# Optimization experiments

Hardware: AMD Instinct MI355X
Metric: run time of the kernel (lower is better)

## Reference

```python
import jax, jax.numpy as jnp
import numpy as np

N_NODES = 100000
N_EDGES = 3200000
N_FEAT = 512
HIDDEN = 16
N_CLASS = 7


def gcn_conv(x, edge_index, W, b, n_nodes):
    """PyG GCNConv (add_self_loops=True, symmetric normalization).
    x: [N, F_in]; edge_index: [2, E] with row=source, col=target.
    """
    h = x @ W  # [N, F_out] -- linear transform before aggregation (F_out small)
    src, dst = edge_index[0], edge_index[1]
    # degree computed on target column (incl. self-loop), as in PyG gcn_norm
    deg = jax.ops.segment_sum(jnp.ones(src.shape[0], dtype=h.dtype), dst,
                              num_segments=n_nodes) + 1.0
    dinv = jax.lax.rsqrt(deg)  # deg >= 1 always (self-loops)
    norm = dinv[src] * dinv[dst]  # [E]
    msg = norm[:, None] * h[src]  # [E, F_out]
    agg = jax.ops.segment_sum(msg, dst, num_segments=n_nodes)
    # self-loop contribution: norm_ii = dinv_i^2
    agg = agg + (dinv * dinv)[:, None] * h
    return agg + b


def setup_inputs() -> dict:
    key = jax.random.key(0)
    k1, k2, k3, k4 = jax.random.split(key, 4)
    x = jax.random.normal(k1, (N_NODES, N_FEAT), dtype=jnp.float32)
    edge_index = jax.random.randint(k2, (2, N_EDGES), 0, N_NODES, dtype=jnp.int64)
    W1 = jax.random.normal(k3, (N_FEAT, HIDDEN), dtype=jnp.float32) * (1.0 / np.sqrt(N_FEAT))
    b1 = jnp.zeros((HIDDEN,), dtype=jnp.float32)
    W2 = jax.random.normal(k4, (HIDDEN, N_CLASS), dtype=jnp.float32) * (1.0 / np.sqrt(HIDDEN))
    b2 = jnp.zeros((N_CLASS,), dtype=jnp.float32)
    return {"x": x, "edge_index": edge_index, "W1": W1, "b1": b1, "W2": W2, "b2": b2}


def reference(x, edge_index, W1, b1, W2, b2):
    n = x.shape[0]
    h = gcn_conv(x, edge_index, W1, b1, n)
    h = jax.nn.relu(h)
    # F.dropout in eval mode is identity (deterministic reference)
    h = gcn_conv(h, edge_index, W2, b2, n)
    return jax.nn.log_softmax(h, axis=1)
```

## Files before the change

kernel.cpp:

```cpp
#include <hip/hip_runtime.h>
#include <math.h>


#define F_IN 512
#define HID  16
#define NCLS 7
#define NCHUNK 256
#define BK 64
#define NBMAX 1600
#define CAP 3072

static __device__ __forceinline__ float bf2f(unsigned short u) {
    union { unsigned int i; float f; } v; v.i = ((unsigned int)u) << 16; return v.f;
}
static __device__ __forceinline__ unsigned short f2bf(float f) {
    union { float f; unsigned int u; } v; v.f = f;
    unsigned int b = v.u;
    return (unsigned short)((b + 0x7FFFu + ((b >> 16) & 1u)) >> 16);
}

__global__ __launch_bounds__(256) void k_a1(const int* __restrict__ ei, int E, int perChunk,
                                            int nb, int* __restrict__ bh) {
    __shared__ int hist[NBMAX];
    for (int t = threadIdx.x; t < nb; t += 256) hist[t] = 0;
    __syncthreads();
    const int* dst = ei + E;
    int c = blockIdx.x;
    int s0 = c * perChunk;
    int s1 = min(s0 + perChunk, E);
    for (int e = s0 + threadIdx.x; e < s1; e += 256)
        atomicAdd(&hist[dst[e] >> 6], 1);
    __syncthreads();
    for (int t = threadIdx.x; t < nb; t += 256) bh[(size_t)c * nb + t] = hist[t];
}

__global__ __launch_bounds__(256) void k_a2a(int* __restrict__ bh, int nb,
                                             int* __restrict__ Tb) {
    __shared__ int sd[256];
    int b = blockIdx.x, tid = threadIdx.x;
    int v = bh[(size_t)tid * nb + b];
    sd[tid] = v;
    __syncthreads();
    for (int off = 1; off < 256; off <<= 1) {
        int t = (tid >= off) ? sd[tid - off] : 0;
        __syncthreads();
        sd[tid] += t;
        __syncthreads();
    }
    bh[(size_t)tid * nb + b] = sd[tid] - v;
    if (tid == 255) Tb[b] = sd[255];
}

__global__ __launch_bounds__(256) void k_a2b(const int* __restrict__ Tb, int nb,
                                             int* __restrict__ Bb) {
    __shared__ int sd[256];
    int tid = threadIdx.x;
    int carry = 0;
    for (int base = 0; base < nb; base += 256) {
        int v = (base + tid < nb) ? Tb[base + tid] : 0;
        sd[tid] = v;
        __syncthreads();
        for (int off = 1; off < 256; off <<= 1) {
            int t = (tid >= off) ? sd[tid - off] : 0;
            __syncthreads();
            sd[tid] += t;
            __syncthreads();
        }
        if (base + tid < nb) Bb[base + tid] = carry + sd[tid] - v;
        carry += sd[255];
        __syncthreads();
    }
}

__global__ __launch_bounds__(256) void k_a3(const int* __restrict__ ei, int E, int perChunk,
                                            int nb, const int* __restrict__ bh,
                                            const int* __restrict__ Bb,
                                            unsigned* __restrict__ part) {
    __shared__ int cur[NBMAX];
    __shared__ int baseL[NBMAX];
    int c = blockIdx.x;
    for (int t = threadIdx.x; t < nb; t += 256) {
        cur[t] = 0;
        baseL[t] = Bb[t] + bh[(size_t)c * nb + t];
    }
    __syncthreads();
    const int* src = ei;
    const int* dst = ei + E;
    int s0 = c * perChunk;
    int s1 = min(s0 + perChunk, E);
    for (int e = s0 + threadIdx.x; e < s1; e += 256) {
        int s = src[e], d = dst[e];
        int b = d >> 6;
        int r = atomicAdd(&cur[b], 1);
        part[baseL[b] + r] = ((unsigned)(d & (BK - 1)) << 20) | (unsigned)s;
    }
}

__global__ __launch_bounds__(256) void k_b(const unsigned* __restrict__ part,
                                           const int* __restrict__ Tb,
                                           const int* __restrict__ Bb,
                                           int* __restrict__ csr, int* __restrict__ cnt,
                                           int* __restrict__ offs, float* __restrict__ dinv,
                                           int N) {
    __shared__ unsigned eL[CAP];
    __shared__ int hist[BK], sd[BK], cur[BK];
    int b = blockIdx.x, tid = threadIdx.x;
    int base = Bb[b], ct = Tb[b];
    if (tid < BK) hist[tid] = 0;
    __syncthreads();
    for (int k = tid; k < ct; k += 256) {
        unsigned v = part[base + k];
        if (k < CAP) eL[k] = v;
        atomicAdd(&hist[v >> 20], 1);
    }
    __syncthreads();
    if (tid < BK) sd[tid] = hist[tid];
    __syncthreads();
    for (int off = 1; off < BK; off <<= 1) {
        int t = 0;
        if (tid < BK && tid >= off) t = sd[tid - off];
        __syncthreads();
        if (tid < BK) sd[tid] += t;
        __syncthreads();
    }
    if (tid < BK) {
        int h = hist[tid];
        int ex = sd[tid] - h;
        cur[tid] = ex;
        int node = b * BK + tid;
        if (node < N) {
            cnt[node] = h;
            offs[node] = base + ex;
            dinv[node] = rsqrtf((float)h + 1.0f);
        }
    }
    __syncthreads();
    for (int k = tid; k < ct; k += 256) {
        unsigned v = (k < CAP) ? eL[k] : part[base + k];
        int dl = (int)(v >> 20);
        int r = atomicAdd(&cur[dl], 1);
        csr[base + r] = (int)(v & 0xFFFFFu);
    }
}

__global__ __launch_bounds__(256) void k_gemm1(const float* __restrict__ x,
                                               const float* __restrict__ W1,
                                               const float* __restrict__ dinv,
                                               unsigned short* __restrict__ hs1b,
                                               int N, int halfN) {
    __shared__ float wl[F_IN * HID];
    for (int t = threadIdx.x; t < F_IN * HID; t += 256) wl[t] = W1[t];
    __syncthreads();
    int gid = blockIdx.x * blockDim.x + threadIdx.x;
    if (gid >= halfN) return;
    int r0 = gid, r1 = gid + halfN;
    bool has1 = (r1 < N);
    const float* x0 = x + (size_t)r0 * F_IN;
    const float* x1 = has1 ? (x + (size_t)r1 * F_IN) : x0;
    float acc0[HID], acc1[HID];
#pragma unroll
    for (int j = 0; j < HID; j++) { acc0[j] = 0.0f; acc1[j] = 0.0f; }
    for (int k0 = 0; k0 < F_IN; k0 += 4) {
        float4 a = *(const float4*)(x0 + k0);
        float4 bq = *(const float4*)(x1 + k0);
        const float* w0 = &wl[k0 * HID];
#pragma unroll
        for (int j = 0; j < HID; j++) {
            float w = w0[j];
            acc0[j] = fmaf(a.x, w, acc0[j]); acc1[j] = fmaf(bq.x, w, acc1[j]);
        }
#pragma unroll
        for (int j = 0; j < HID; j++) {
            float w = w0[HID + j];
            acc0[j] = fmaf(a.y, w, acc0[j]); acc1[j] = fmaf(bq.y, w, acc1[j]);
        }
#pragma unroll
        for (int j = 0; j < HID; j++) {
            float w = w0[2 * HID + j];
            acc0[j] = fmaf(a.z, w, acc0[j]); acc1[j] = fmaf(bq.z, w, acc1[j]);
        }
#pragma unroll
        for (int j = 0; j < HID; j++) {
            float w = w0[3 * HID + j];
            acc0[j] = fmaf(a.w, w, acc0[j]); acc1[j] = fmaf(bq.w, w, acc1[j]);
        }
    }
    float d0 = dinv[r0];
    unsigned p0[8];
#pragma unroll
    for (int j = 0; j < 8; j++) {
        unsigned lo = f2bf(d0 * acc0[2 * j]);
        unsigned hi = f2bf(d0 * acc0[2 * j + 1]);
        p0[j] = lo | (hi << 16);
    }
    *(uint4*)(hs1b + (size_t)r0 * HID)     = make_uint4(p0[0], p0[1], p0[2], p0[3]);
    *(uint4*)(hs1b + (size_t)r0 * HID + 8) = make_uint4(p0[4], p0[5], p0[6], p0[7]);
    if (has1) {
        float d1 = dinv[r1];
        unsigned p1[8];
#pragma unroll
        for (int j = 0; j < 8; j++) {
            unsigned lo = f2bf(d1 * acc1[2 * j]);
            unsigned hi = f2bf(d1 * acc1[2 * j + 1]);
            p1[j] = lo | (hi << 16);
        }
        *(uint4*)(hs1b + (size_t)r1 * HID)     = make_uint4(p1[0], p1[1], p1[2], p1[3]);
        *(uint4*)(hs1b + (size_t)r1 * HID + 8) = make_uint4(p1[4], p1[5], p1[6], p1[7]);
    }
}

__global__ __launch_bounds__(256) void k_agg1(const int* __restrict__ csr,
                                              const int* __restrict__ offs,
                                              const int* __restrict__ cnt,
                                              const float* __restrict__ dinv,
                                              const unsigned short* __restrict__ hs1b,
                                              const float* __restrict__ b1,
                                              const float* __restrict__ W2,
                                              float* __restrict__ hs2, int N) {
    int lane = threadIdx.x & 15;
    int i = blockIdx.x * 16 + (threadIdx.x >> 4);
    float w2r[NCLS];
#pragma unroll
    for (int c = 0; c < NCLS; c++) w2r[c] = W2[lane * NCLS + c];
    float b1l = b1[lane];
    if (i >= N) return;
    int start = offs[i], end = start + cnt[i];
    float acc = bf2f(hs1b[(size_t)i * HID + lane]);
    int k = start;
    for (; k + 3 < end; k += 4) {
        int s0 = csr[k], s1 = csr[k + 1], s2 = csr[k + 2], s3 = csr[k + 3];
        float v0 = bf2f(hs1b[(size_t)s0 * HID + lane]);
        float v1 = bf2f(hs1b[(size_t)s1 * HID + lane]);
        float v2 = bf2f(hs1b[(size_t)s2 * HID + lane]);
        float v3 = bf2f(hs1b[(size_t)s3 * HID + lane]);
        acc += (v0 + v1) + (v2 + v3);
    }
    for (; k < end; k++)
        acc += bf2f(hs1b[(size_t)csr[k] * HID + lane]);
    float v = fmaf(dinv[i], acc, b1l);
    float hr = v > 0.0f ? v : 0.0f;
    float dv = dinv[i];
    float res[NCLS];
#pragma unroll
    for (int c = 0; c < NCLS; c++) {
        float t = hr * w2r[c];
#pragma unroll
        for (int w = 8; w >= 1; w >>= 1) t += __shfl_xor(t, w, 16);
        res[c] = t;
    }
    if (lane < NCLS) {
        float o = res[0];
#pragma unroll
        for (int c = 1; c < NCLS; c++) o = (lane == c) ? res[c] : o;
        hs2[(size_t)i * NCLS + lane] = dv * o;
    }
}

__global__ __launch_bounds__(256) void k_agg2(const int* __restrict__ csr,
                                              const int* __restrict__ offs,
                                              const int* __restrict__ cnt,
                                              const float* __restrict__ dinv,
                                              const float* __restrict__ hs2,
                                              const float* __restrict__ b2,
                                              float* __restrict__ out, int N) {
    int lane = threadIdx.x & 7;
    int i = blockIdx.x * 32 + (threadIdx.x >> 3);
    if (i >= N) return;
    int cc = lane < NCLS ? lane : NCLS - 1;
    int start = offs[i], end = start + cnt[i];
    float acc = hs2[(size_t)i * NCLS + cc];
    int k = start;
    for (; k + 3 < end; k += 4) {
        int s0 = csr[k], s1 = csr[k + 1], s2 = csr[k + 2], s3 = csr[k + 3];
        float v0 = hs2[(size_t)s0 * NCLS + cc];
        float v1 = hs2[(size_t)s1 * NCLS + cc];
        float v2 = hs2[(size_t)s2 * NCLS + cc];
        float v3 = hs2[(size_t)s3 * NCLS + cc];
        acc += (v0 + v1) + (v2 + v3);
    }
    for (; k < end; k++)
        acc += hs2[(size_t)csr[k] * NCLS + cc];
    float v = fmaf(dinv[i], acc, b2[cc]);
    float vm = (lane < NCLS) ? v : -INFINITY;
    float m = vm;
#pragma unroll
    for (int w = 4; w >= 1; w >>= 1) m = fmaxf(m, __shfl_xor(m, w, 8));
    float e = (lane < NCLS) ? expf(v - m) : 0.0f;
    float ssum = e;
#pragma unroll
    for (int w = 4; w >= 1; w >>= 1) ssum += __shfl_xor(ssum, w, 8);
    if (lane < NCLS) out[(size_t)i * NCLS + lane] = v - m - logf(ssum);
}

extern "C" void kernel_launch(void* const* d_in, const int* in_sizes, int n_in,
                              void* d_out, int out_size, void* d_ws, size_t ws_size,
                              hipStream_t stream) {
    const float* x  = (const float*)d_in[0];
    const int*   ei = (const int*)d_in[1];
    const float* W1 = (const float*)d_in[2];
    const float* b1 = (const float*)d_in[3];
    const float* W2 = (const float*)d_in[4];
    const float* b2 = (const float*)d_in[5];
    float* out = (float*)d_out;

    const int N = in_sizes[0] / F_IN;
    const int E = in_sizes[1] / 2;
    const int nb = (N + BK - 1) / BK;
    const int halfN = (N + 1) / 2;
    const int perChunk = (E + NCHUNK - 1) / NCHUNK;

    unsigned* w = (unsigned*)d_ws;
    auto al4 = [](size_t v) { return (v + 3) & ~(size_t)3; };
    size_t o = 0;
    unsigned*       part = w + o;               o = al4(o + E);
    int*            csr  = (int*)(w + o);       o = al4(o + E);
    unsigned short* hs1b = (unsigned short*)(w + o); o = al4(o + (size_t)N * HID / 2);
    float*          hs2  = (float*)(w + o);     o = al4(o + (size_t)N * NCLS);
    float*          dinv = (float*)(w + o);     o = al4(o + N);
    int*            cnt  = (int*)(w + o);       o = al4(o + N);
    int*            offs = (int*)(w + o);       o = al4(o + N);
    int*            bh   = (int*)(w + o);       o = al4(o + (size_t)NCHUNK * nb);
    int*            Tb   = (int*)(w + o);       o = al4(o + nb);
    int*            Bb   = (int*)(w + o);

    k_a1<<<NCHUNK, 256, 0, stream>>>(ei, E, perChunk, nb, bh);
    k_a2a<<<nb, 256, 0, stream>>>(bh, nb, Tb);
    k_a2b<<<1, 256, 0, stream>>>(Tb, nb, Bb);
    k_a3<<<NCHUNK, 256, 0, stream>>>(ei, E, perChunk, nb, bh, Bb, part);
    k_b<<<nb, 256, 0, stream>>>(part, Tb, Bb, csr, cnt, offs, dinv, N);
    k_gemm1<<<(halfN + 255) / 256, 256, 0, stream>>>(x, W1, dinv, hs1b, N, halfN);
    k_agg1<<<(N + 15) / 16, 256, 0, stream>>>(csr, offs, cnt, dinv, hs1b, b1, W2, hs2, N);
    k_agg2<<<(N + 31) / 32, 256, 0, stream>>>(csr, offs, cnt, dinv, hs2, b2, out, N);
}
```

Before: 513.8 us.

## Restructure GEMM1 so 16-lane groups split K with coalesced row loads

The first linear layer now assigns 16 lanes to each group of 4 rows. Each lane reads a contiguous float4 slice of the row and multiplies it against a transposed, padded copy of W1 in shared memory. Partial sums are combined with a butterfly shuffle reduction that leaves one output column per lane. This replaces one-thread-per-two-rows loads, which strided 2KB per lane, with coalesced accesses to the large x matrix. The cost is shuffle-reduction overhead and scalar bf16 stores, plus a messy host-side workspace layout recomputation.

Result: faster. 486.7 us (-5.3%).

```diff
diff --git a/kernel.cpp b/kernel.cpp
--- a/kernel.cpp
+++ b/kernel.cpp
@@ -9,6 +9,7 @@
 #define BK 64
 #define NBMAX 1600
 #define CAP 3072
+#define WT_STRIDE 516
 
 static __device__ __forceinline__ float bf2f(unsigned short u) {
     union { unsigned int i; float f; } v; v.i = ((unsigned int)u) << 16; return v.f;
@@ -147,65 +148,83 @@
                                                const float* __restrict__ W1,
                                                const float* __restrict__ dinv,
                                                unsigned short* __restrict__ hs1b,
-                                               int N, int halfN) {
-    __shared__ float wl[F_IN * HID];
-    for (int t = threadIdx.x; t < F_IN * HID; t += 256) wl[t] = W1[t];
-    __syncthreads();
-    int gid = blockIdx.x * blockDim.x + threadIdx.x;
-    if (gid >= halfN) return;
-    int r0 = gid, r1 = gid + halfN;
-    bool has1 = (r1 < N);
-    const float* x0 = x + (size_t)r0 * F_IN;
-    const float* x1 = has1 ? (x + (size_t)r1 * F_IN) : x0;
-    float acc0[HID], acc1[HID];
-#pragma unroll
-    for (int j = 0; j < HID; j++) { acc0[j] = 0.0f; acc1[j] = 0.0f; }
-    for (int k0 = 0; k0 < F_IN; k0 += 4) {
-        float4 a = *(const float4*)(x0 + k0);
-        float4 bq = *(const float4*)(x1 + k0);
-        const float* w0 = &wl[k0 * HID];
-#pragma unroll
-        for (int j = 0; j < HID; j++) {
-            float w = w0[j];
-            acc0[j] = fmaf(a.x, w, acc0[j]); acc1[j] = fmaf(bq.x, w, acc1[j]);
-        }
-#pragma unroll
-        for (int j = 0; j < HID; j++) {
-            float w = w0[HID + j];
-            acc0[j] = fmaf(a.y, w, acc0[j]); acc1[j] = fmaf(bq.y, w, acc1[j]);
-        }
-#pragma unroll
-        for (int j = 0; j < HID; j++) {
-            float w = w0[2 * HID + j];
-            acc0[j] = fmaf(a.z, w, acc0[j]); acc1[j] = fmaf(bq.z, w, acc1[j]);
-        }
-#pragma unroll
-        for (int j = 0; j < HID; j++) {
-            float w = w0[3 * HID + j];
-            acc0[j] = fmaf(a.w, w, acc0[j]); acc1[j] = fmaf(bq.w, w, acc1[j]);
-        }
-    }
-    float d0 = dinv[r0];
-    unsigned p0[8];
-#pragma unroll
-    for (int j = 0; j < 8; j++) {
-        unsigned lo = f2bf(d0 * acc0[2 * j]);
-        unsigned hi = f2bf(d0 * acc0[2 * j + 1]);
-        p0[j] = lo | (hi << 16);
-    }
-    *(uint4*)(hs1b + (size_t)r0 * HID)     = make_uint4(p0[0], p0[1], p0[2], p0[3]);
-    *(uint4*)(hs1b + (size_t)r0 * HID + 8) = make_uint4(p0[4], p0[5], p0[6], p0[7]);
-    if (has1) {
-        float d1 = dinv[r1];
-        unsigned p1[8];
-#pragma unroll
-        for (int j = 0; j < 8; j++) {
-            unsigned lo = f2bf(d1 * acc1[2 * j]);
-            unsigned hi = f2bf(d1 * acc1[2 * j + 1]);
-            p1[j] = lo | (hi << 16);
-        }
-        *(uint4*)(hs1b + (size_t)r1 * HID)     = make_uint4(p1[0], p1[1], p1[2], p1[3]);
-        *(uint4*)(hs1b + (size_t)r1 * HID + 8) = make_uint4(p1[4], p1[5], p1[6], p1[7]);
+                                               int N) {
+    __shared__ float wlT[HID * WT_STRIDE];
+    {
+        int j = threadIdx.x & 15;
+        int k0 = threadIdx.x >> 4;
+        for (int it = 0; it < F_IN / 16; ++it) {
+            int k = k0 + 16 * it;
+            wlT[j * WT_STRIDE + k] = W1[k * HID + j];
+        }
+    }
+    __syncthreads();
+
+    int lane = threadIdx.x & 15;
+    int g = threadIdx.x >> 4;
+    int rbase = blockIdx.x * 64 + g * 4;
+
+    const float* xp0 = x + (size_t)(rbase + 0 < N ? rbase + 0 : 0) * F_IN + 4 * lane;
+    const float* xp1 = x + (size_t)(rbase + 1 < N ? rbase + 1 : 0) * F_IN + 4 * lane;
+    const float* xp2 = x + (size_t)(rbase + 2 < N ? rbase + 2 : 0) * F_IN + 4 * lane;
+    const float* xp3 = x + (size_t)(rbase + 3 < N ? rbase + 3 : 0) * F_IN + 4 * lane;
+
+    float acc[4][16];
+#pragma unroll
+    for (int r = 0; r < 4; ++r)
+#pragma unroll
+        for (int j = 0; j < 16; ++j) acc[r][j] = 0.0f;
+
+#pragma unroll 2
+    for (int p = 0; p < 8; ++p) {
+        float4 a0 = *(const float4*)(xp0 + 64 * p);
+        float4 a1 = *(const float4*)(xp1 + 64 * p);
+        float4 a2 = *(const float4*)(xp2 + 64 * p);
+        float4 a3 = *(const float4*)(xp3 + 64 * p);
+        const float* wb = &wlT[64 * p + 4 * lane];
+#pragma unroll
+        for (int j = 0; j < 16; ++j) {
+            float4 w4 = *(const float4*)(wb + (size_t)j * WT_STRIDE);
+            acc[0][j] = fmaf(a0.x, w4.x, fmaf(a0.y, w4.y, fmaf(a0.z, w4.z, fmaf(a0.w, w4.w, acc[0][j]))));
+            acc[1][j] = fmaf(a1.x, w4.x, fmaf(a1.y, w4.y, fmaf(a1.z, w4.z, fmaf(a1.w, w4.w, acc[1][j]))));
+            acc[2][j] = fmaf(a2.x, w4.x, fmaf(a2.y, w4.y, fmaf(a2.z, w4.z, fmaf(a2.w, w4.w, acc[2][j]))));
+            acc[3][j] = fmaf(a3.x, w4.x, fmaf(a3.y, w4.y, fmaf(a3.z, w4.z, fmaf(a3.w, w4.w, acc[3][j]))));
+        }
+    }
+
+    bool b8 = (lane & 8) != 0, b4 = (lane & 4) != 0, b2 = (lane & 2) != 0, b1 = (lane & 1) != 0;
+#pragma unroll
+    for (int r = 0; r < 4; ++r) {
+#pragma unroll
+        for (int j = 0; j < 8; ++j) {
+            float lo = acc[r][j], hi = acc[r][j + 8];
+            float keep = b8 ? hi : lo;
+            float send = b8 ? lo : hi;
+            acc[r][j] = keep + __shfl_xor(send, 8, 16);
+        }
+#pragma unroll
+        for (int j = 0; j < 4; ++j) {
+            float lo = acc[r][j], hi = acc[r][j + 4];
+            float keep = b4 ? hi : lo;
+            float send = b4 ? lo : hi;
+            acc[r][j] = keep + __shfl_xor(send, 4, 16);
+        }
+#pragma unroll
+        for (int j = 0; j < 2; ++j) {
+            float lo = acc[r][j], hi = acc[r][j + 2];
+            float keep = b2 ? hi : lo;
+            float send = b2 ? lo : hi;
+            acc[r][j] = keep + __shfl_xor(send, 2, 16);
+        }
+        {
+            float lo = acc[r][0], hi = acc[r][1];
+            float keep = b1 ? hi : lo;
+            float send = b1 ? lo : hi;
+            acc[r][0] = keep + __shfl_xor(send, 1, 16);
+        }
+        int row = rbase + r;
+        if (row < N)
+            hs1b[(size_t)row * HID + lane] = f2bf(dinv[row] * acc[r][0]);
     }
 }
 
@@ -306,7 +325,6 @@
     const int N = in_sizes[0] / F_IN;
     const int E = in_sizes[1] / 2;
     const int nb = (N + BK - 1) / BK;
-    const int halfN = (N + 1) / 2;
     const int perChunk = (E + NCHUNK - 1) / NCHUNK;
 
     unsigned* w = (unsigned*)d_ws;
@@ -318,7 +336,15 @@
     float*          hs2  = (float*)(w + o);     o = al4(o + (size_t)N * NCLS);
     float*          dinv = (float*)(w + o);     o = al4(o + N);
     int*            cnt  = (int*)(w + o);       o = al4(o + N);
-    int*            offs = (int*)(w + o);       o = al4(o + N);
+    int*            offs = (int*)(w + o);       o = al4(o + (size_t)NCHUNK * nb > 0 ? o + N - N + N : N), o = al4(o);
+    o = 0;
+    part = w + o;                               o = al4(o + E);
+    csr  = (int*)(w + o);                       o = al4(o + E);
+    hs1b = (unsigned short*)(w + o);            o = al4(o + (size_t)N * HID / 2);
+    hs2  = (float*)(w + o);                     o = al4(o + (size_t)N * NCLS);
+    dinv = (float*)(w + o);                     o = al4(o + N);
+    cnt  = (int*)(w + o);                       o = al4(o + N);
+    offs = (int*)(w + o);                       o = al4(o + N);
     int*            bh   = (int*)(w + o);       o = al4(o + (size_t)NCHUNK * nb);
     int*            Tb   = (int*)(w + o);       o = al4(o + nb);
     int*            Bb   = (int*)(w + o);
@@ -328,7 +354,7 @@
     k_a2b<<<1, 256, 0, stream>>>(Tb, nb, Bb);
     k_a3<<<NCHUNK, 256, 0, stream>>>(ei, E, perChunk, nb, bh, Bb, part);
     k_b<<<nb, 256, 0, stream>>>(part, Tb, Bb, csr, cnt, offs, dinv, N);
-    k_gemm1<<<(halfN + 255) / 256, 256, 0, stream>>>(x, W1, dinv, hs1b, N, halfN);
+    k_gemm1<<<(N + 63) / 64, 256, 0, stream>>>(x, W1, dinv, hs1b, N);
     k_agg1<<<(N + 15) / 16, 256, 0, stream>>>(csr, offs, cnt, dinv, hs1b, b1, W2, hs2, N);
     k_agg2<<<(N + 31) / 32, 256, 0, stream>>>(csr, offs, cnt, dinv, hs2, b2, out, N);
 }
```
